# Kernel optimization log

Hardware: AMD Instinct MI355X
Metric: run time of the kernel (lower is better)

Reference implementation:

```python
import jax, jax.numpy as jnp
import numpy as np

B, T, C, H = 8, 2048, 1024, 64

def setup_inputs() -> dict:
    key = jax.random.key(0)
    k1, k2, k3, k4 = jax.random.split(key, 4)
    sc = 1.0 / np.sqrt(C)
    return {
        "x": jax.random.normal(k1, (B, T, C), dtype=jnp.float32),
        "Wk": jax.random.normal(k2, (C, H), dtype=jnp.float32) * sc,
        "Wq": jax.random.normal(k3, (C, H), dtype=jnp.float32) * sc,
        "Wv": jax.random.normal(k4, (C, H), dtype=jnp.float32) * sc,
    }

def reference(x, Wk, Wq, Wv):
    # bias-free projections: [B,T,C] @ [C,H] -> [B,T,H]
    k = jnp.einsum("btc,ch->bth", x, Wk)
    q = jnp.einsum("btc,ch->bth", x, Wq)
    v = jnp.einsum("btc,ch->bth", x, Wv)
    scale = Wk.shape[-1] ** -0.5  # head_size ** -0.5
    # attention scores [B,T,T]
    wei = jnp.einsum("bth,bsh->bts", q, k) * scale
    # causal mask: position t attends to s <= t
    Tn = x.shape[1]
    causal = jnp.tril(jnp.ones((Tn, Tn), dtype=bool))
    wei = jnp.where(causal[None, :, :], wei, jnp.float32(-jnp.inf))
    wei = jax.nn.softmax(wei, axis=-1)
    out = jnp.einsum("bts,bsh->bth", wei, v)  # [B,T,H]
    return out
```

## Files before the change

kernel.cpp:

```cpp
#include <hip/hip_runtime.h>
#include <math.h>

#define Bb 8
#define Tt 2048
#define Cc 1024
#define Hh 64

typedef __attribute__((ext_vector_type(8))) short short8;
typedef __attribute__((ext_vector_type(4))) float f32x4;

static __device__ __forceinline__ unsigned short f2bf(float f) {
    union { float f; unsigned u; } v; v.f = f;
    return (unsigned short)((v.u + 0x7FFFu + ((v.u >> 16) & 1u)) >> 16);
}

#define LOG2E 1.44269504088896340736f

__global__ __launch_bounds__(256)
void wconv_kernel(const float* __restrict__ Wk, const float* __restrict__ Wq,
                  const float* __restrict__ Wv, unsigned short* __restrict__ WbT)
{
    const int n = blockIdx.x;
    const int h = n & 63;
    const float* W; float scale = 1.0f;
    if (n < 64)       { W = Wq; scale = 0.125f * LOG2E; }
    else if (n < 128) { W = Wk; }
    else              { W = Wv; }
    #pragma unroll
    for (int i = 0; i < 4; ++i) {
        const int k = threadIdx.x + (i << 8);
        WbT[n * 1024 + k] = f2bf(W[k * 64 + h] * scale);
    }
}

__global__ __launch_bounds__(256)
void proj_kernel(const float* __restrict__ x, const unsigned short* __restrict__ WbT,
                 unsigned short* __restrict__ qb, unsigned short* __restrict__ kb,
                 unsigned short* __restrict__ vt)
{
    __shared__ unsigned short As[32][72];
    __shared__ unsigned short Bs[192][72];

    const int tid  = threadIdx.x;
    const int row0 = blockIdx.x * 32;
    const int lane = tid & 63;
    const int w    = tid >> 6;
    const int fr   = lane & 15;
    const int fg   = lane >> 4;
    const int fko  = fg << 3;

    f32x4 acc[2][3];
    #pragma unroll
    for (int i = 0; i < 2; ++i)
        #pragma unroll
        for (int j = 0; j < 3; ++j) acc[i][j] = (f32x4){0.f, 0.f, 0.f, 0.f};

    for (int k0 = 0; k0 < Cc; k0 += 64) {
        {
            const int r  = tid >> 3;
            const int ko = (tid & 7) << 3;
            const float* src = &x[(size_t)(row0 + r) * Cc + k0 + ko];
            const float4 a0 = *reinterpret_cast<const float4*>(src);
            const float4 a1 = *reinterpret_cast<const float4*>(src + 4);
            short8 h8;
            h8[0] = (short)f2bf(a0.x); h8[1] = (short)f2bf(a0.y);
            h8[2] = (short)f2bf(a0.z); h8[3] = (short)f2bf(a0.w);
            h8[4] = (short)f2bf(a1.x); h8[5] = (short)f2bf(a1.y);
            h8[6] = (short)f2bf(a1.z); h8[7] = (short)f2bf(a1.w);
            *reinterpret_cast<short8*>(&As[r][ko]) = h8;
        }
        #pragma unroll
        for (int i = 0; i < 6; ++i) {
            const int c  = tid + (i << 8);
            const int r  = c >> 3;
            const int ko = (c & 7) << 3;
            *reinterpret_cast<short8*>(&Bs[r][ko]) =
                *reinterpret_cast<const short8*>(&WbT[(size_t)r * 1024 + k0 + ko]);
        }
        __syncthreads();

        #pragma unroll
        for (int sub = 0; sub < 2; ++sub) {
            short8 af[2], bf[3];
            #pragma unroll
            for (int mf = 0; mf < 2; ++mf)
                af[mf] = *reinterpret_cast<const short8*>(
                    &As[mf * 16 + fr][sub * 32 + fko]);
            #pragma unroll
            for (int nf = 0; nf < 3; ++nf)
                bf[nf] = *reinterpret_cast<const short8*>(
                    &Bs[w * 48 + nf * 16 + fr][sub * 32 + fko]);
            #pragma unroll
            for (int mf = 0; mf < 2; ++mf)
                #pragma unroll
                for (int nf = 0; nf < 3; ++nf)
                    acc[mf][nf] = __builtin_amdgcn_mfma_f32_16x16x32_bf16(
                        af[mf], bf[nf], acc[mf][nf], 0, 0, 0);
        }
        __syncthreads();
    }

    #pragma unroll
    for (int mf = 0; mf < 2; ++mf)
        #pragma unroll
        for (int nf = 0; nf < 3; ++nf) {
            const int col  = w * 48 + nf * 16 + fr;
            const int mat  = col >> 6;
            const int h    = col & 63;
            const int rowb = row0 + mf * 16 + (fg << 2);
            if (mat == 2) {
                const int bb = rowb >> 11;
                const int t  = rowb & 2047;
                ushort4 pk;
                pk.x = f2bf(acc[mf][nf][0]); pk.y = f2bf(acc[mf][nf][1]);
                pk.z = f2bf(acc[mf][nf][2]); pk.w = f2bf(acc[mf][nf][3]);
                *reinterpret_cast<ushort4*>(&vt[((size_t)bb * 64 + h) * Tt + t]) = pk;
            } else {
                unsigned short* dst = mat ? kb : qb;
                #pragma unroll
                for (int r = 0; r < 4; ++r)
                    dst[(size_t)(rowb + r) * 64 + h] = f2bf(acc[mf][nf][r]);
            }
        }
}

__global__ __launch_bounds__(256)
void attn_kernel(const unsigned short* __restrict__ qb,
                 const unsigned short* __restrict__ kb,
                 const unsigned short* __restrict__ vt,
                 float* __restrict__ out)
{
    __shared__ float smem[9216];

    const int tid  = threadIdx.x;
    const int fid  = blockIdx.x;
    const int b    = fid & 7;
    const int qt   = 63 - (fid >> 3);
    const int lane = tid & 63;
    const int w    = tid >> 6;
    const int fr   = lane & 15;
    const int fg   = lane >> 4;
    const int fko  = fg << 3;
    const int ktmax = qt >> 1;

    short8 aq[2][2];
    #pragma unroll
    for (int n = 0; n < 2; ++n)
        #pragma unroll
        for (int hs = 0; hs < 2; ++hs) {
            const size_t gq = (size_t)b * Tt + qt * 32 + n * 16 + fr;
            aq[n][hs] = *reinterpret_cast<const short8*>(&qb[gq * 64 + hs * 32 + fko]);
        }

    float mrun[2] = {-INFINITY, -INFINITY}, lrun[2] = {0.f, 0.f};
    f32x4 O[2][4];
    #pragma unroll
    for (int mf = 0; mf < 2; ++mf)
        #pragma unroll
        for (int nh = 0; nh < 4; ++nh) O[mf][nh] = (f32x4){0.f, 0.f, 0.f, 0.f};

    unsigned short* Pw = (unsigned short*)smem + w * 2304;

    for (int kt = w; kt <= ktmax; kt += 4) {
        short8 bk[4][2], bv[4][2];
        #pragma unroll
        for (int kf = 0; kf < 4; ++kf)
            #pragma unroll
            for (int hs = 0; hs < 2; ++hs) {
                const size_t gk = (size_t)b * Tt + kt * 64 + kf * 16 + fr;
                bk[kf][hs] = *reinterpret_cast<const short8*>(&kb[gk * 64 + hs * 32 + fko]);
            }
        #pragma unroll
        for (int nh = 0; nh < 4; ++nh)
            #pragma unroll
            for (int ks = 0; ks < 2; ++ks) {
                const size_t gv = ((size_t)b * 64 + nh * 16 + fr) * Tt
                                  + kt * 64 + ks * 32 + fko;
                bv[nh][ks] = *reinterpret_cast<const short8*>(&vt[gv]);
            }

        const f32x4 zero = (f32x4){0.f, 0.f, 0.f, 0.f};
        f32x4 st[4][2];
        #pragma unroll
        for (int kf = 0; kf < 4; ++kf)
            #pragma unroll
            for (int n = 0; n < 2; ++n) {
                f32x4 t = __builtin_amdgcn_mfma_f32_16x16x32_bf16(bk[kf][0], aq[n][0], zero, 0, 0, 0);
                st[kf][n] = __builtin_amdgcn_mfma_f32_16x16x32_bf16(bk[kf][1], aq[n][1], t, 0, 0, 0);
            }

        if (kt == ktmax) {
            #pragma unroll
            for (int kf = 0; kf < 4; ++kf)
                #pragma unroll
                for (int n = 0; n < 2; ++n)
                    #pragma unroll
                    for (int r = 0; r < 4; ++r) {
                        const int key  = kt * 64 + kf * 16 + (fg << 2) + r;
                        const int qrow = qt * 32 + n * 16 + fr;
                        if (key > qrow) st[kf][n][r] = -INFINITY;
                    }
        }

        float alpha[2];
        #pragma unroll
        for (int n = 0; n < 2; ++n) {
            float tmax = -INFINITY;
            #pragma unroll
            for (int kf = 0; kf < 4; ++kf)
                #pragma unroll
                for (int r = 0; r < 4; ++r) tmax = fmaxf(tmax, st[kf][n][r]);
            tmax = fmaxf(tmax, __shfl_xor(tmax, 16, 64));
            tmax = fmaxf(tmax, __shfl_xor(tmax, 32, 64));
            const float mn = fmaxf(mrun[n], tmax);
            const float al = exp2f(mrun[n] - mn);
            float psum = 0.f;
            #pragma unroll
            for (int kf = 0; kf < 4; ++kf)
                #pragma unroll
                for (int r = 0; r < 4; ++r) {
                    const float pv = exp2f(st[kf][n][r] - mn);
                    st[kf][n][r] = pv;
                    psum += pv;
                }
            psum += __shfl_xor(psum, 16, 64);
            psum += __shfl_xor(psum, 32, 64);
            lrun[n] = lrun[n] * al + psum;
            mrun[n] = mn;
            alpha[n] = al;
        }

        #pragma unroll
        for (int kf = 0; kf < 4; ++kf)
            #pragma unroll
            for (int n = 0; n < 2; ++n) {
                ushort4 pk;
                pk.x = f2bf(st[kf][n][0]); pk.y = f2bf(st[kf][n][1]);
                pk.z = f2bf(st[kf][n][2]); pk.w = f2bf(st[kf][n][3]);
                *reinterpret_cast<ushort4*>(
                    &Pw[(n * 16 + fr) * 72 + kf * 16 + (fg << 2)]) = pk;
            }

        #pragma unroll
        for (int mf = 0; mf < 2; ++mf) {
            f32x4 av;
            #pragma unroll
            for (int r = 0; r < 4; ++r)
                av[r] = __shfl(alpha[mf], (fg << 2) + r, 64);
            #pragma unroll
            for (int nh = 0; nh < 4; ++nh) O[mf][nh] *= av;
        }

        short8 pa[2][2];
        #pragma unroll
        for (int mf = 0; mf < 2; ++mf)
            #pragma unroll
            for (int ks = 0; ks < 2; ++ks)
                pa[mf][ks] = *reinterpret_cast<const short8*>(
                    &Pw[(mf * 16 + fr) * 72 + ks * 32 + fko]);
        #pragma unroll
        for (int mf = 0; mf < 2; ++mf)
            #pragma unroll
            for (int nh = 0; nh < 4; ++nh) {
                O[mf][nh] = __builtin_amdgcn_mfma_f32_16x16x32_bf16(pa[mf][0], bv[nh][0], O[mf][nh], 0, 0, 0);
                O[mf][nh] = __builtin_amdgcn_mfma_f32_16x16x32_bf16(pa[mf][1], bv[nh][1], O[mf][nh], 0, 0, 0);
            }
    }

    __syncthreads();
    float* Om = smem;
    float* Ms = smem + 8704;
    float* Ls = smem + 8832;
    #pragma unroll
    for (int mf = 0; mf < 2; ++mf)
        #pragma unroll
        for (int nh = 0; nh < 4; ++nh)
            #pragma unroll
            for (int r = 0; r < 4; ++r)
                Om[(w * 32 + mf * 16 + (fg << 2) + r) * 68 + nh * 16 + fr] = O[mf][nh][r];
    if (fg == 0) {
        #pragma unroll
        for (int n = 0; n < 2; ++n) {
            Ms[w * 32 + n * 16 + fr] = mrun[n];
            Ls[w * 32 + n * 16 + fr] = lrun[n];
        }
    }
    __syncthreads();

    const int row = tid >> 3;
    const int h0  = (tid & 7) << 3;
    float M = -INFINITY;
    #pragma unroll
    for (int ww = 0; ww < 4; ++ww) M = fmaxf(M, Ms[ww * 32 + row]);
    float L = 0.f, o[8];
    #pragma unroll
    for (int j = 0; j < 8; ++j) o[j] = 0.f;
    #pragma unroll
    for (int ww = 0; ww < 4; ++ww) {
        const float sc = exp2f(Ms[ww * 32 + row] - M);
        L += Ls[ww * 32 + row] * sc;
        const float4 a = *reinterpret_cast<const float4*>(&Om[(ww * 32 + row) * 68 + h0]);
        const float4 c = *reinterpret_cast<const float4*>(&Om[(ww * 32 + row) * 68 + h0 + 4]);
        o[0] += a.x * sc; o[1] += a.y * sc; o[2] += a.z * sc; o[3] += a.w * sc;
        o[4] += c.x * sc; o[5] += c.y * sc; o[6] += c.z * sc; o[7] += c.w * sc;
    }
    const float invL = 1.f / L;
    float* dst = &out[((size_t)b * Tt + qt * 32 + row) * 64 + h0];
    *reinterpret_cast<float4*>(dst)     = make_float4(o[0]*invL, o[1]*invL, o[2]*invL, o[3]*invL);
    *reinterpret_cast<float4*>(dst + 4) = make_float4(o[4]*invL, o[5]*invL, o[6]*invL, o[7]*invL);
}

extern "C" void kernel_launch(void* const* d_in, const int* in_sizes, int n_in,
                              void* d_out, int out_size, void* d_ws, size_t ws_size,
                              hipStream_t stream)
{
    const float* x  = (const float*)d_in[0];
    const float* Wk = (const float*)d_in[1];
    const float* Wq = (const float*)d_in[2];
    const float* Wv = (const float*)d_in[3];
    float* out = (float*)d_out;

    const size_t n = (size_t)Bb * Tt * Hh;
    unsigned short* WbT = (unsigned short*)d_ws;
    unsigned short* qb  = WbT + 196608;
    unsigned short* kb  = qb + n;
    unsigned short* vt  = kb + n;

    wconv_kernel<<<dim3(192), 256, 0, stream>>>(Wk, Wq, Wv, WbT);
    proj_kernel <<<dim3(512), 256, 0, stream>>>(x, WbT, qb, kb, vt);
    attn_kernel <<<dim3(512), 256, 0, stream>>>(qb, kb, vt, out);
}
```

Measured before the change: 140.5 us.

## Halve attention query tile, prefetch x in projection, use hardware bf16 pack

The attention kernel now processes 16 query rows per block instead of 32, doubling the grid to 1024 blocks. It also skips the rescale of O when no wave lane's max changes, and sets launch bounds for 4 blocks per CU. The projection kernel drops the shared-memory staging of weights, reads B fragments straight from global, and register-prefetches the next x tile. Conversions use the v_cvt_pk_bf16_f32 instruction. Smaller query tiles give more parallelism and less register pressure, but halve reuse of K/V loads per block.

Result: slower. 161.3 us (+14.8%).

```diff
diff --git a/kernel.cpp b/kernel.cpp
--- a/kernel.cpp
+++ b/kernel.cpp
@@ -12,6 +12,11 @@
 static __device__ __forceinline__ unsigned short f2bf(float f) {
     union { float f; unsigned u; } v; v.f = f;
     return (unsigned short)((v.u + 0x7FFFu + ((v.u >> 16) & 1u)) >> 16);
+}
+static __device__ __forceinline__ unsigned pack2(float lo, float hi) {
+    unsigned r;
+    asm("v_cvt_pk_bf16_f32 %0, %1, %2" : "=v"(r) : "v"(lo), "v"(hi));
+    return r;
 }
 
 #define LOG2E 1.44269504088896340736f
@@ -39,7 +44,6 @@
                  unsigned short* __restrict__ vt)
 {
     __shared__ unsigned short As[32][72];
-    __shared__ unsigned short Bs[192][72];
 
     const int tid  = threadIdx.x;
     const int row0 = blockIdx.x * 32;
@@ -49,36 +53,36 @@
     const int fg   = lane >> 4;
     const int fko  = fg << 3;
 
+    const int ar = tid >> 3;
+    const int ac = (tid & 7) << 3;
+    const float* xrow = &x[(size_t)(row0 + ar) * Cc + ac];
+
+    const unsigned short* Brow[3];
+    #pragma unroll
+    for (int nf = 0; nf < 3; ++nf)
+        Brow[nf] = &WbT[(size_t)(w * 48 + nf * 16 + fr) * 1024 + fko];
+
     f32x4 acc[2][3];
     #pragma unroll
     for (int i = 0; i < 2; ++i)
         #pragma unroll
         for (int j = 0; j < 3; ++j) acc[i][j] = (f32x4){0.f, 0.f, 0.f, 0.f};
 
-    for (int k0 = 0; k0 < Cc; k0 += 64) {
-        {
-            const int r  = tid >> 3;
-            const int ko = (tid & 7) << 3;
-            const float* src = &x[(size_t)(row0 + r) * Cc + k0 + ko];
-            const float4 a0 = *reinterpret_cast<const float4*>(src);
-            const float4 a1 = *reinterpret_cast<const float4*>(src + 4);
-            short8 h8;
-            h8[0] = (short)f2bf(a0.x); h8[1] = (short)f2bf(a0.y);
-            h8[2] = (short)f2bf(a0.z); h8[3] = (short)f2bf(a0.w);
-            h8[4] = (short)f2bf(a1.x); h8[5] = (short)f2bf(a1.y);
-            h8[6] = (short)f2bf(a1.z); h8[7] = (short)f2bf(a1.w);
-            *reinterpret_cast<short8*>(&As[r][ko]) = h8;
-        }
-        #pragma unroll
-        for (int i = 0; i < 6; ++i) {
-            const int c  = tid + (i << 8);
-            const int r  = c >> 3;
-            const int ko = (c & 7) << 3;
-            *reinterpret_cast<short8*>(&Bs[r][ko]) =
-                *reinterpret_cast<const short8*>(&WbT[(size_t)r * 1024 + k0 + ko]);
-        }
-        __syncthreads();
-
+    {
+        const float4 a0 = *reinterpret_cast<const float4*>(xrow);
+        const float4 a1 = *reinterpret_cast<const float4*>(xrow + 4);
+        *reinterpret_cast<uint4*>(&As[ar][ac]) =
+            make_uint4(pack2(a0.x, a0.y), pack2(a0.z, a0.w),
+                       pack2(a1.x, a1.y), pack2(a1.z, a1.w));
+    }
+    __syncthreads();
+
+    for (int t = 0; t < 16; ++t) {
+        float4 n0, n1;
+        if (t < 15) {
+            n0 = *reinterpret_cast<const float4*>(xrow + (t + 1) * 64);
+            n1 = *reinterpret_cast<const float4*>(xrow + (t + 1) * 64 + 4);
+        }
         #pragma unroll
         for (int sub = 0; sub < 2; ++sub) {
             short8 af[2], bf[3];
@@ -89,13 +93,19 @@
             #pragma unroll
             for (int nf = 0; nf < 3; ++nf)
                 bf[nf] = *reinterpret_cast<const short8*>(
-                    &Bs[w * 48 + nf * 16 + fr][sub * 32 + fko]);
+                    &Brow[nf][t * 64 + sub * 32]);
             #pragma unroll
             for (int mf = 0; mf < 2; ++mf)
                 #pragma unroll
                 for (int nf = 0; nf < 3; ++nf)
                     acc[mf][nf] = __builtin_amdgcn_mfma_f32_16x16x32_bf16(
                         af[mf], bf[nf], acc[mf][nf], 0, 0, 0);
+        }
+        __syncthreads();
+        if (t < 15) {
+            *reinterpret_cast<uint4*>(&As[ar][ac]) =
+                make_uint4(pack2(n0.x, n0.y), pack2(n0.z, n0.w),
+                           pack2(n1.x, n1.y), pack2(n1.z, n1.w));
         }
         __syncthreads();
     }
@@ -111,10 +121,10 @@
             if (mat == 2) {
                 const int bb = rowb >> 11;
                 const int t  = rowb & 2047;
-                ushort4 pk;
-                pk.x = f2bf(acc[mf][nf][0]); pk.y = f2bf(acc[mf][nf][1]);
-                pk.z = f2bf(acc[mf][nf][2]); pk.w = f2bf(acc[mf][nf][3]);
-                *reinterpret_cast<ushort4*>(&vt[((size_t)bb * 64 + h) * Tt + t]) = pk;
+                uint2 pk;
+                pk.x = pack2(acc[mf][nf][0], acc[mf][nf][1]);
+                pk.y = pack2(acc[mf][nf][2], acc[mf][nf][3]);
+                *reinterpret_cast<uint2*>(&vt[((size_t)bb * 64 + h) * Tt + t]) = pk;
             } else {
                 unsigned short* dst = mat ? kb : qb;
                 #pragma unroll
@@ -124,52 +134,52 @@
         }
 }
 
-__global__ __launch_bounds__(256)
+__global__ __launch_bounds__(256, 4)
 void attn_kernel(const unsigned short* __restrict__ qb,
                  const unsigned short* __restrict__ kb,
                  const unsigned short* __restrict__ vt,
                  float* __restrict__ out)
 {
-    __shared__ float smem[9216];
+    __shared__ float smem[4608];
 
     const int tid  = threadIdx.x;
     const int fid  = blockIdx.x;
     const int b    = fid & 7;
-    const int qt   = 63 - (fid >> 3);
+    const int qt   = 127 - (fid >> 3);
     const int lane = tid & 63;
     const int w    = tid >> 6;
     const int fr   = lane & 15;
     const int fg   = lane >> 4;
     const int fko  = fg << 3;
-    const int ktmax = qt >> 1;
-
-    short8 aq[2][2];
-    #pragma unroll
-    for (int n = 0; n < 2; ++n)
-        #pragma unroll
-        for (int hs = 0; hs < 2; ++hs) {
-            const size_t gq = (size_t)b * Tt + qt * 32 + n * 16 + fr;
-            aq[n][hs] = *reinterpret_cast<const short8*>(&qb[gq * 64 + hs * 32 + fko]);
-        }
-
-    float mrun[2] = {-INFINITY, -INFINITY}, lrun[2] = {0.f, 0.f};
-    f32x4 O[2][4];
-    #pragma unroll
-    for (int mf = 0; mf < 2; ++mf)
-        #pragma unroll
-        for (int nh = 0; nh < 4; ++nh) O[mf][nh] = (f32x4){0.f, 0.f, 0.f, 0.f};
-
-    unsigned short* Pw = (unsigned short*)smem + w * 2304;
+    const int ktmax = qt >> 2;
+
+    short8 aq[2];
+    #pragma unroll
+    for (int hs = 0; hs < 2; ++hs) {
+        const size_t gq = (size_t)b * Tt + qt * 16 + fr;
+        aq[hs] = *reinterpret_cast<const short8*>(&qb[gq * 64 + hs * 32 + fko]);
+    }
+
+    float mrun = -INFINITY, lrun = 0.f;
+    f32x4 O[4];
+    #pragma unroll
+    for (int nh = 0; nh < 4; ++nh) O[nh] = (f32x4){0.f, 0.f, 0.f, 0.f};
+
+    unsigned short* Pw = (unsigned short*)smem + w * 1152;
 
     for (int kt = w; kt <= ktmax; kt += 4) {
-        short8 bk[4][2], bv[4][2];
-        #pragma unroll
-        for (int kf = 0; kf < 4; ++kf)
-            #pragma unroll
-            for (int hs = 0; hs < 2; ++hs) {
-                const size_t gk = (size_t)b * Tt + kt * 64 + kf * 16 + fr;
-                bk[kf][hs] = *reinterpret_cast<const short8*>(&kb[gk * 64 + hs * 32 + fko]);
-            }
+        const f32x4 zero = (f32x4){0.f, 0.f, 0.f, 0.f};
+        f32x4 st[4];
+        #pragma unroll
+        for (int kf = 0; kf < 4; ++kf) {
+            const size_t gk = (size_t)b * Tt + kt * 64 + kf * 16 + fr;
+            const short8 k0 = *reinterpret_cast<const short8*>(&kb[gk * 64 + fko]);
+            const short8 k1 = *reinterpret_cast<const short8*>(&kb[gk * 64 + 32 + fko]);
+            f32x4 t = __builtin_amdgcn_mfma_f32_16x16x32_bf16(k0, aq[0], zero, 0, 0, 0);
+            st[kf]  = __builtin_amdgcn_mfma_f32_16x16x32_bf16(k1, aq[1], t, 0, 0, 0);
+        }
+
+        short8 bv[4][2];
         #pragma unroll
         for (int nh = 0; nh < 4; ++nh)
             #pragma unroll
@@ -179,135 +189,101 @@
                 bv[nh][ks] = *reinterpret_cast<const short8*>(&vt[gv]);
             }
 
-        const f32x4 zero = (f32x4){0.f, 0.f, 0.f, 0.f};
-        f32x4 st[4][2];
-        #pragma unroll
-        for (int kf = 0; kf < 4; ++kf)
-            #pragma unroll
-            for (int n = 0; n < 2; ++n) {
-                f32x4 t = __builtin_amdgcn_mfma_f32_16x16x32_bf16(bk[kf][0], aq[n][0], zero, 0, 0, 0);
-                st[kf][n] = __builtin_amdgcn_mfma_f32_16x16x32_bf16(bk[kf][1], aq[n][1], t, 0, 0, 0);
-            }
-
         if (kt == ktmax) {
-            #pragma unroll
-            for (int kf = 0; kf < 4; ++kf)
-                #pragma unroll
-                for (int n = 0; n < 2; ++n)
-                    #pragma unroll
-                    for (int r = 0; r < 4; ++r) {
-                        const int key  = kt * 64 + kf * 16 + (fg << 2) + r;
-                        const int qrow = qt * 32 + n * 16 + fr;
-                        if (key > qrow) st[kf][n][r] = -INFINITY;
-                    }
-        }
-
-        float alpha[2];
-        #pragma unroll
-        for (int n = 0; n < 2; ++n) {
-            float tmax = -INFINITY;
-            #pragma unroll
-            for (int kf = 0; kf < 4; ++kf)
-                #pragma unroll
-                for (int r = 0; r < 4; ++r) tmax = fmaxf(tmax, st[kf][n][r]);
-            tmax = fmaxf(tmax, __shfl_xor(tmax, 16, 64));
-            tmax = fmaxf(tmax, __shfl_xor(tmax, 32, 64));
-            const float mn = fmaxf(mrun[n], tmax);
-            const float al = exp2f(mrun[n] - mn);
-            float psum = 0.f;
             #pragma unroll
             for (int kf = 0; kf < 4; ++kf)
                 #pragma unroll
                 for (int r = 0; r < 4; ++r) {
-                    const float pv = exp2f(st[kf][n][r] - mn);
-                    st[kf][n][r] = pv;
-                    psum += pv;
+                    const int key  = kt * 64 + kf * 16 + (fg << 2) + r;
+                    const int qrow = qt * 16 + fr;
+                    if (key > qrow) st[kf][r] = -INFINITY;
                 }
-            psum += __shfl_xor(psum, 16, 64);
-            psum += __shfl_xor(psum, 32, 64);
-            lrun[n] = lrun[n] * al + psum;
-            mrun[n] = mn;
-            alpha[n] = al;
-        }
-
+        }
+
+        float t0 = fmaxf(fmaxf(st[0][0], st[0][1]), fmaxf(st[0][2], st[0][3]));
+        float t1 = fmaxf(fmaxf(st[1][0], st[1][1]), fmaxf(st[1][2], st[1][3]));
+        float t2 = fmaxf(fmaxf(st[2][0], st[2][1]), fmaxf(st[2][2], st[2][3]));
+        float t3 = fmaxf(fmaxf(st[3][0], st[3][1]), fmaxf(st[3][2], st[3][3]));
+        float tmax = fmaxf(fmaxf(t0, t1), fmaxf(t2, t3));
+        tmax = fmaxf(tmax, __shfl_xor(tmax, 16, 64));
+        tmax = fmaxf(tmax, __shfl_xor(tmax, 32, 64));
+        const float mn = fmaxf(mrun, tmax);
+        if (__any(mn > mrun)) {
+            const float al = exp2f(mrun - mn);
+            float av[4];
+            #pragma unroll
+            for (int r = 0; r < 4; ++r)
+                av[r] = __shfl(al, (fg << 2) + r, 64);
+            const f32x4 avv = (f32x4){av[0], av[1], av[2], av[3]};
+            #pragma unroll
+            for (int nh = 0; nh < 4; ++nh) O[nh] *= avv;
+            lrun *= al;
+            mrun = mn;
+        }
+        float psum = 0.f;
         #pragma unroll
         for (int kf = 0; kf < 4; ++kf)
             #pragma unroll
-            for (int n = 0; n < 2; ++n) {
-                ushort4 pk;
-                pk.x = f2bf(st[kf][n][0]); pk.y = f2bf(st[kf][n][1]);
-                pk.z = f2bf(st[kf][n][2]); pk.w = f2bf(st[kf][n][3]);
-                *reinterpret_cast<ushort4*>(
-                    &Pw[(n * 16 + fr) * 72 + kf * 16 + (fg << 2)]) = pk;
+            for (int r = 0; r < 4; ++r) {
+                const float pv = exp2f(st[kf][r] - mrun);
+                st[kf][r] = pv;
+                psum += pv;
             }
-
-        #pragma unroll
-        for (int mf = 0; mf < 2; ++mf) {
-            f32x4 av;
-            #pragma unroll
-            for (int r = 0; r < 4; ++r)
-                av[r] = __shfl(alpha[mf], (fg << 2) + r, 64);
-            #pragma unroll
-            for (int nh = 0; nh < 4; ++nh) O[mf][nh] *= av;
-        }
-
-        short8 pa[2][2];
-        #pragma unroll
-        for (int mf = 0; mf < 2; ++mf)
-            #pragma unroll
-            for (int ks = 0; ks < 2; ++ks)
-                pa[mf][ks] = *reinterpret_cast<const short8*>(
-                    &Pw[(mf * 16 + fr) * 72 + ks * 32 + fko]);
-        #pragma unroll
-        for (int mf = 0; mf < 2; ++mf)
-            #pragma unroll
-            for (int nh = 0; nh < 4; ++nh) {
-                O[mf][nh] = __builtin_amdgcn_mfma_f32_16x16x32_bf16(pa[mf][0], bv[nh][0], O[mf][nh], 0, 0, 0);
-                O[mf][nh] = __builtin_amdgcn_mfma_f32_16x16x32_bf16(pa[mf][1], bv[nh][1], O[mf][nh], 0, 0, 0);
-            }
+        psum += __shfl_xor(psum, 16, 64);
+        psum += __shfl_xor(psum, 32, 64);
+        lrun += psum;
+
+        #pragma unroll
+        for (int kf = 0; kf < 4; ++kf) {
+            uint2 pk;
+            pk.x = pack2(st[kf][0], st[kf][1]);
+            pk.y = pack2(st[kf][2], st[kf][3]);
+            *reinterpret_cast<uint2*>(&Pw[fr * 72 + kf * 16 + (fg << 2)]) = pk;
+        }
+
+        short8 pa[2];
+        #pragma unroll
+        for (int ks = 0; ks < 2; ++ks)
+            pa[ks] = *reinterpret_cast<const short8*>(&Pw[fr * 72 + ks * 32 + fko]);
+        #pragma unroll
+        for (int nh = 0; nh < 4; ++nh) {
+            O[nh] = __builtin_amdgcn_mfma_f32_16x16x32_bf16(pa[0], bv[nh][0], O[nh], 0, 0, 0);
+            O[nh] = __builtin_amdgcn_mfma_f32_16x16x32_bf16(pa[1], bv[nh][1], O[nh], 0, 0, 0);
+        }
     }
 
     __syncthreads();
     float* Om = smem;
-    float* Ms = smem + 8704;
-    float* Ls = smem + 8832;
-    #pragma unroll
-    for (int mf = 0; mf < 2; ++mf)
-        #pragma unroll
-        for (int nh = 0; nh < 4; ++nh)
-            #pragma unroll
-            for (int r = 0; r < 4; ++r)
-                Om[(w * 32 + mf * 16 + (fg << 2) + r) * 68 + nh * 16 + fr] = O[mf][nh][r];
+    float* Ms = smem + 4352;
+    float* Ls = smem + 4416;
+    #pragma unroll
+    for (int nh = 0; nh < 4; ++nh)
+        #pragma unroll
+        for (int r = 0; r < 4; ++r)
+            Om[(w * 16 + (fg << 2) + r) * 68 + nh * 16 + fr] = O[nh][r];
     if (fg == 0) {
-        #pragma unroll
-        for (int n = 0; n < 2; ++n) {
-            Ms[w * 32 + n * 16 + fr] = mrun[n];
-            Ls[w * 32 + n * 16 + fr] = lrun[n];
-        }
+        Ms[w * 16 + fr] = mrun;
+        Ls[w * 16 + fr] = lrun;
     }
     __syncthreads();
 
-    const int row = tid >> 3;
-    const int h0  = (tid & 7) << 3;
+    const int row = tid >> 4;
+    const int h0  = (tid & 15) << 2;
     float M = -INFINITY;
     #pragma unroll
-    for (int ww = 0; ww < 4; ++ww) M = fmaxf(M, Ms[ww * 32 + row]);
-    float L = 0.f, o[8];
-    #pragma unroll
-    for (int j = 0; j < 8; ++j) o[j] = 0.f;
+    for (int ww = 0; ww < 4; ++ww) M = fmaxf(M, Ms[ww * 16 + row]);
+    float L = 0.f;
+    float4 o = make_float4(0.f, 0.f, 0.f, 0.f);
     #pragma unroll
     for (int ww = 0; ww < 4; ++ww) {
-        const float sc = exp2f(Ms[ww * 32 + row] - M);
-        L += Ls[ww * 32 + row] * sc;
-        const float4 a = *reinterpret_cast<const float4*>(&Om[(ww * 32 + row) * 68 + h0]);
-        const float4 c = *reinterpret_cast<const float4*>(&Om[(ww * 32 + row) * 68 + h0 + 4]);
-        o[0] += a.x * sc; o[1] += a.y * sc; o[2] += a.z * sc; o[3] += a.w * sc;
-        o[4] += c.x * sc; o[5] += c.y * sc; o[6] += c.z * sc; o[7] += c.w * sc;
+        const float sc = exp2f(Ms[ww * 16 + row] - M);
+        L += Ls[ww * 16 + row] * sc;
+        const float4 a = *reinterpret_cast<const float4*>(&Om[(ww * 16 + row) * 68 + h0]);
+        o.x += a.x * sc; o.y += a.y * sc; o.z += a.z * sc; o.w += a.w * sc;
     }
     const float invL = 1.f / L;
-    float* dst = &out[((size_t)b * Tt + qt * 32 + row) * 64 + h0];
-    *reinterpret_cast<float4*>(dst)     = make_float4(o[0]*invL, o[1]*invL, o[2]*invL, o[3]*invL);
-    *reinterpret_cast<float4*>(dst + 4) = make_float4(o[4]*invL, o[5]*invL, o[6]*invL, o[7]*invL);
+    *reinterpret_cast<float4*>(&out[((size_t)b * Tt + qt * 16 + row) * 64 + h0]) =
+        make_float4(o.x * invL, o.y * invL, o.z * invL, o.w * invL);
 }
 
 extern "C" void kernel_launch(void* const* d_in, const int* in_sizes, int n_in,
@@ -326,7 +302,7 @@
     unsigned short* kb  = qb + n;
     unsigned short* vt  = kb + n;
 
-    wconv_kernel<<<dim3(192), 256, 0, stream>>>(Wk, Wq, Wv, WbT);
-    proj_kernel <<<dim3(512), 256, 0, stream>>>(x, WbT, qb, kb, vt);
-    attn_kernel <<<dim3(512), 256, 0, stream>>>(qb, kb, vt, out);
-}
+    wconv_kernel<<<dim3(192),  256, 0, stream>>>(Wk, Wq, Wv, WbT);
+    proj_kernel <<<dim3(512),  256, 0, stream>>>(x, WbT, qb, kb, vt);
+    attn_kernel <<<dim3(1024), 256, 0, stream>>>(qb, kb, vt, out);
+}
```

## Stage full x row block in LDS, prefetch K tiles, skip redundant rescale

Applied to the files above, without the earlier changes.

The projection kernel now converts the whole 32x1024 x tile to bf16 into LDS once and reads weights directly from global memory, which removes the per-chunk syncthreads and the B-tile staging. The attention kernel double-buffers K fragments so the next tile loads while the current one is computed. It also skips the O/l rescaling when no row max increased in the wave, uses the packed v_cvt_pk_bf16_f32 conversion, and adds a launch_bounds occupancy hint. The larger LDS footprint (about 65KB) may limit proj occupancy, and the extra prefetch registers may add pressure.

After: 146.7 us. 1.04x slower.

```diff
diff --git a/kernel.cpp b/kernel.cpp
--- a/kernel.cpp
+++ b/kernel.cpp
@@ -12,6 +12,11 @@
 static __device__ __forceinline__ unsigned short f2bf(float f) {
     union { float f; unsigned u; } v; v.f = f;
     return (unsigned short)((v.u + 0x7FFFu + ((v.u >> 16) & 1u)) >> 16);
+}
+static __device__ __forceinline__ unsigned pack2(float lo, float hi) {
+    unsigned r;
+    asm("v_cvt_pk_bf16_f32 %0, %1, %2" : "=v"(r) : "v"(lo), "v"(hi));
+    return r;
 }
 
 #define LOG2E 1.44269504088896340736f
@@ -33,13 +38,13 @@
     }
 }
 
+#define PK 1040
 __global__ __launch_bounds__(256)
 void proj_kernel(const float* __restrict__ x, const unsigned short* __restrict__ WbT,
                  unsigned short* __restrict__ qb, unsigned short* __restrict__ kb,
                  unsigned short* __restrict__ vt)
 {
-    __shared__ unsigned short As[32][72];
-    __shared__ unsigned short Bs[192][72];
+    __shared__ unsigned short As[32 * PK];
 
     const int tid  = threadIdx.x;
     const int row0 = blockIdx.x * 32;
@@ -49,47 +54,46 @@
     const int fg   = lane >> 4;
     const int fko  = fg << 3;
 
+    {
+        const int ar = tid >> 3;
+        const int ac = (tid & 7) << 3;
+        const float* xrow = &x[(size_t)(row0 + ar) * Cc + ac];
+        unsigned short* dstA = &As[ar * PK + ac];
+        #pragma unroll
+        for (int c = 0; c < 16; ++c) {
+            const float4 a0 = *reinterpret_cast<const float4*>(xrow + c * 64);
+            const float4 a1 = *reinterpret_cast<const float4*>(xrow + c * 64 + 4);
+            *reinterpret_cast<uint4*>(dstA + c * 64) =
+                make_uint4(pack2(a0.x, a0.y), pack2(a0.z, a0.w),
+                           pack2(a1.x, a1.y), pack2(a1.z, a1.w));
+        }
+    }
+    __syncthreads();
+
+    const unsigned short* Brow[3];
+    #pragma unroll
+    for (int nf = 0; nf < 3; ++nf)
+        Brow[nf] = &WbT[(size_t)(w * 48 + nf * 16 + fr) * 1024 + fko];
+
     f32x4 acc[2][3];
     #pragma unroll
     for (int i = 0; i < 2; ++i)
         #pragma unroll
         for (int j = 0; j < 3; ++j) acc[i][j] = (f32x4){0.f, 0.f, 0.f, 0.f};
 
-    for (int k0 = 0; k0 < Cc; k0 += 64) {
-        {
-            const int r  = tid >> 3;
-            const int ko = (tid & 7) << 3;
-            const float* src = &x[(size_t)(row0 + r) * Cc + k0 + ko];
-            const float4 a0 = *reinterpret_cast<const float4*>(src);
-            const float4 a1 = *reinterpret_cast<const float4*>(src + 4);
-            short8 h8;
-            h8[0] = (short)f2bf(a0.x); h8[1] = (short)f2bf(a0.y);
-            h8[2] = (short)f2bf(a0.z); h8[3] = (short)f2bf(a0.w);
-            h8[4] = (short)f2bf(a1.x); h8[5] = (short)f2bf(a1.y);
-            h8[6] = (short)f2bf(a1.z); h8[7] = (short)f2bf(a1.w);
-            *reinterpret_cast<short8*>(&As[r][ko]) = h8;
-        }
-        #pragma unroll
-        for (int i = 0; i < 6; ++i) {
-            const int c  = tid + (i << 8);
-            const int r  = c >> 3;
-            const int ko = (c & 7) << 3;
-            *reinterpret_cast<short8*>(&Bs[r][ko]) =
-                *reinterpret_cast<const short8*>(&WbT[(size_t)r * 1024 + k0 + ko]);
-        }
-        __syncthreads();
-
+    #pragma unroll 4
+    for (int t = 0; t < 16; ++t) {
         #pragma unroll
         for (int sub = 0; sub < 2; ++sub) {
             short8 af[2], bf[3];
             #pragma unroll
             for (int mf = 0; mf < 2; ++mf)
                 af[mf] = *reinterpret_cast<const short8*>(
-                    &As[mf * 16 + fr][sub * 32 + fko]);
+                    &As[(mf * 16 + fr) * PK + t * 64 + sub * 32 + fko]);
             #pragma unroll
             for (int nf = 0; nf < 3; ++nf)
                 bf[nf] = *reinterpret_cast<const short8*>(
-                    &Bs[w * 48 + nf * 16 + fr][sub * 32 + fko]);
+                    &Brow[nf][t * 64 + sub * 32]);
             #pragma unroll
             for (int mf = 0; mf < 2; ++mf)
                 #pragma unroll
@@ -97,7 +101,6 @@
                     acc[mf][nf] = __builtin_amdgcn_mfma_f32_16x16x32_bf16(
                         af[mf], bf[nf], acc[mf][nf], 0, 0, 0);
         }
-        __syncthreads();
     }
 
     #pragma unroll
@@ -111,10 +114,10 @@
             if (mat == 2) {
                 const int bb = rowb >> 11;
                 const int t  = rowb & 2047;
-                ushort4 pk;
-                pk.x = f2bf(acc[mf][nf][0]); pk.y = f2bf(acc[mf][nf][1]);
-                pk.z = f2bf(acc[mf][nf][2]); pk.w = f2bf(acc[mf][nf][3]);
-                *reinterpret_cast<ushort4*>(&vt[((size_t)bb * 64 + h) * Tt + t]) = pk;
+                uint2 pk;
+                pk.x = pack2(acc[mf][nf][0], acc[mf][nf][1]);
+                pk.y = pack2(acc[mf][nf][2], acc[mf][nf][3]);
+                *reinterpret_cast<uint2*>(&vt[((size_t)bb * 64 + h) * Tt + t]) = pk;
             } else {
                 unsigned short* dst = mat ? kb : qb;
                 #pragma unroll
@@ -124,7 +127,7 @@
         }
 }
 
-__global__ __launch_bounds__(256)
+__global__ __launch_bounds__(256, 2)
 void attn_kernel(const unsigned short* __restrict__ qb,
                  const unsigned short* __restrict__ kb,
                  const unsigned short* __restrict__ vt,
@@ -161,15 +164,16 @@
 
     unsigned short* Pw = (unsigned short*)smem + w * 2304;
 
-    for (int kt = w; kt <= ktmax; kt += 4) {
-        short8 bk[4][2], bv[4][2];
+    auto body = [&](int kt, short8 (&CUR)[4][2], short8 (&NXT)[4][2]) {
+        const int ktn = (kt + 4 <= ktmax) ? kt + 4 : ktmax;
         #pragma unroll
         for (int kf = 0; kf < 4; ++kf)
             #pragma unroll
             for (int hs = 0; hs < 2; ++hs) {
-                const size_t gk = (size_t)b * Tt + kt * 64 + kf * 16 + fr;
-                bk[kf][hs] = *reinterpret_cast<const short8*>(&kb[gk * 64 + hs * 32 + fko]);
-            }
+                const size_t gk = (size_t)b * Tt + ktn * 64 + kf * 16 + fr;
+                NXT[kf][hs] = *reinterpret_cast<const short8*>(&kb[gk * 64 + hs * 32 + fko]);
+            }
+        short8 bv[4][2];
         #pragma unroll
         for (int nh = 0; nh < 4; ++nh)
             #pragma unroll
@@ -185,8 +189,8 @@
         for (int kf = 0; kf < 4; ++kf)
             #pragma unroll
             for (int n = 0; n < 2; ++n) {
-                f32x4 t = __builtin_amdgcn_mfma_f32_16x16x32_bf16(bk[kf][0], aq[n][0], zero, 0, 0, 0);
-                st[kf][n] = __builtin_amdgcn_mfma_f32_16x16x32_bf16(bk[kf][1], aq[n][1], t, 0, 0, 0);
+                f32x4 t = __builtin_amdgcn_mfma_f32_16x16x32_bf16(CUR[kf][0], aq[n][0], zero, 0, 0, 0);
+                st[kf][n] = __builtin_amdgcn_mfma_f32_16x16x32_bf16(CUR[kf][1], aq[n][1], t, 0, 0, 0);
             }
 
         if (kt == ktmax) {
@@ -202,7 +206,7 @@
                     }
         }
 
-        float alpha[2];
+        float mn[2];
         #pragma unroll
         for (int n = 0; n < 2; ++n) {
             float tmax = -INFINITY;
@@ -212,44 +216,52 @@
                 for (int r = 0; r < 4; ++r) tmax = fmaxf(tmax, st[kf][n][r]);
             tmax = fmaxf(tmax, __shfl_xor(tmax, 16, 64));
             tmax = fmaxf(tmax, __shfl_xor(tmax, 32, 64));
-            const float mn = fmaxf(mrun[n], tmax);
-            const float al = exp2f(mrun[n] - mn);
+            mn[n] = fmaxf(mrun[n], tmax);
+        }
+        if (__any((mn[0] > mrun[0]) | (mn[1] > mrun[1]))) {
+            float alpha[2];
+            #pragma unroll
+            for (int n = 0; n < 2; ++n) {
+                alpha[n] = exp2f(mrun[n] - mn[n]);
+                lrun[n] *= alpha[n];
+                mrun[n] = mn[n];
+            }
+            #pragma unroll
+            for (int mf = 0; mf < 2; ++mf) {
+                f32x4 av;
+                #pragma unroll
+                for (int r = 0; r < 4; ++r)
+                    av[r] = __shfl(alpha[mf], (fg << 2) + r, 64);
+                #pragma unroll
+                for (int nh = 0; nh < 4; ++nh) O[mf][nh] *= av;
+            }
+        }
+        #pragma unroll
+        for (int n = 0; n < 2; ++n) {
             float psum = 0.f;
             #pragma unroll
             for (int kf = 0; kf < 4; ++kf)
                 #pragma unroll
                 for (int r = 0; r < 4; ++r) {
-                    const float pv = exp2f(st[kf][n][r] - mn);
+                    const float pv = exp2f(st[kf][n][r] - mrun[n]);
                     st[kf][n][r] = pv;
                     psum += pv;
                 }
             psum += __shfl_xor(psum, 16, 64);
             psum += __shfl_xor(psum, 32, 64);
-            lrun[n] = lrun[n] * al + psum;
-            mrun[n] = mn;
-            alpha[n] = al;
+            lrun[n] += psum;
         }
 
         #pragma unroll
         for (int kf = 0; kf < 4; ++kf)
             #pragma unroll
             for (int n = 0; n < 2; ++n) {
-                ushort4 pk;
-                pk.x = f2bf(st[kf][n][0]); pk.y = f2bf(st[kf][n][1]);
-                pk.z = f2bf(st[kf][n][2]); pk.w = f2bf(st[kf][n][3]);
-                *reinterpret_cast<ushort4*>(
+                uint2 pk;
+                pk.x = pack2(st[kf][n][0], st[kf][n][1]);
+                pk.y = pack2(st[kf][n][2], st[kf][n][3]);
+                *reinterpret_cast<uint2*>(
                     &Pw[(n * 16 + fr) * 72 + kf * 16 + (fg << 2)]) = pk;
             }
-
-        #pragma unroll
-        for (int mf = 0; mf < 2; ++mf) {
-            f32x4 av;
-            #pragma unroll
-            for (int r = 0; r < 4; ++r)
-                av[r] = __shfl(alpha[mf], (fg << 2) + r, 64);
-            #pragma unroll
-            for (int nh = 0; nh < 4; ++nh) O[mf][nh] *= av;
-        }
 
         short8 pa[2][2];
         #pragma unroll
@@ -265,6 +277,21 @@
                 O[mf][nh] = __builtin_amdgcn_mfma_f32_16x16x32_bf16(pa[mf][0], bv[nh][0], O[mf][nh], 0, 0, 0);
                 O[mf][nh] = __builtin_amdgcn_mfma_f32_16x16x32_bf16(pa[mf][1], bv[nh][1], O[mf][nh], 0, 0, 0);
             }
+    };
+
+    short8 bkA[4][2], bkB[4][2];
+    if (w <= ktmax) {
+        #pragma unroll
+        for (int kf = 0; kf < 4; ++kf)
+            #pragma unroll
+            for (int hs = 0; hs < 2; ++hs) {
+                const size_t gk = (size_t)b * Tt + w * 64 + kf * 16 + fr;
+                bkA[kf][hs] = *reinterpret_cast<const short8*>(&kb[gk * 64 + hs * 32 + fko]);
+            }
+        for (int kt = w; kt <= ktmax; kt += 8) {
+            body(kt, bkA, bkB);
+            if (kt + 4 <= ktmax) body(kt + 4, bkB, bkA);
+        }
     }
 
     __syncthreads();
```
